# Kernel tuning notes

Measured on AMD Instinct MI355X. Metric: run time of the kernel, lower is better.

## Reference

```python
import jax, jax.numpy as jnp
import numpy as np

N = 100000          # total nodes
E = 1600000         # edges
C = 128             # in_channels
H = 256             # hidden_size
ACT_DIM = 20        # nodes per graph -> batch = N // ACT_DIM


def setup_inputs() -> dict:
    key = jax.random.key(0)
    ks = jax.random.split(key, 10)
    x = jax.random.normal(ks[0], (N, C), dtype=jnp.float32)
    edge_index = jax.random.randint(ks[1], (2, E), 0, N, dtype=jnp.int64)
    s = 0.05
    conv_w = jax.random.normal(ks[2], (C, C), dtype=jnp.float32) * s   # [in, out]
    conv_b = jnp.zeros((C,), dtype=jnp.float32)
    lin1_w = jax.random.normal(ks[3], (H, C), dtype=jnp.float32) * s   # torch [out, in]
    lin1_b = jnp.zeros((H,), dtype=jnp.float32)
    lin2_w = jax.random.normal(ks[4], (H, H), dtype=jnp.float32) * s
    lin2_b = jnp.zeros((H,), dtype=jnp.float32)
    lin3_w = jax.random.normal(ks[5], (1, H), dtype=jnp.float32) * s
    lin3_b = jnp.zeros((1,), dtype=jnp.float32)
    return {"x": x, "edge_index": edge_index,
            "conv_w": conv_w, "conv_b": conv_b,
            "lin1_w": lin1_w, "lin1_b": lin1_b,
            "lin2_w": lin2_w, "lin2_b": lin2_b,
            "lin3_w": lin3_w, "lin3_b": lin3_b}


def gcn_conv(x, edge_index, w, b):
    """PyG GCNConv: x' = D^{-1/2} (A + I) D^{-1/2} (x W) + b."""
    n = x.shape[0]
    loops = jnp.arange(n, dtype=edge_index.dtype)
    src = jnp.concatenate([edge_index[0], loops])  # [E + N]
    dst = jnp.concatenate([edge_index[1], loops])
    deg = jax.ops.segment_sum(jnp.ones_like(dst, dtype=x.dtype), dst, num_segments=n)
    dinv = jnp.where(deg > 0, jax.lax.rsqrt(deg), 0.0)
    norm = dinv[src] * dinv[dst]                   # [E + N]
    xw = x @ w                                     # [N, out]
    msg = xw[src] * norm[:, None]                  # gather + scale, [E+N, out]
    out = jax.ops.segment_sum(msg, dst, num_segments=n)  # scatter-add
    return out + b


def reference(x, edge_index, conv_w, conv_b, lin1_w, lin1_b, lin2_w, lin2_b, lin3_w, lin3_b):
    out = jax.nn.relu(gcn_conv(x, edge_index, conv_w, conv_b))
    h = out + x                                    # residual, [N, C]
    h = h.reshape(-1, ACT_DIM, C)                  # [B, act_dim, C]
    h = jax.nn.relu(h @ lin1_w.T + lin1_b)         # [B, act_dim, H]
    h = jax.nn.relu(h @ lin2_w.T + lin2_b)
    h = jnp.sum(h, axis=1)                         # [B, H]
    h = h @ lin3_w.T + lin3_b                      # [B, 1]
    if h.shape[0] == 1:                            # torch .squeeze(0) semantics
        h = h[0]
    return h
```

## Files before the change

### kernel.cpp

```cpp
#include <hip/hip_runtime.h>
#include <hip/hip_bf16.h>
#include <cstddef>

#define NNODES 100000
#define NEDGES 1600000
#define CIN 128
#define HID 256
#define ACT 20
#define NGRAPH (NNODES / ACT)
#define BSHIFT 8
#define NB ((NNODES + 255) >> 8)
#define BIN_WGS 512
#define PER_WG (NEDGES / BIN_WGS)
#define CAP 8192
#define NSLICE 8
#define PLANE ((size_t)NNODES * 16)

typedef __attribute__((ext_vector_type(8))) short short8;
typedef __attribute__((ext_vector_type(4))) float f32x4;

__device__ __forceinline__ unsigned short f2b(float f) {
    unsigned u = __float_as_uint(f);
    u += 0x7FFF + ((u >> 16) & 1);
    return (unsigned short)(u >> 16);
}
__device__ __forceinline__ float b2f(unsigned short h) {
    return __uint_as_float(((unsigned)h) << 16);
}


__global__ __launch_bounds__(256) void bin_k(const int* __restrict__ ei,
                                             int* __restrict__ bfill,
                                             unsigned* __restrict__ entries) {
    __shared__ int cnt[NB], lofs[NB], base[NB], cur[NB];
    __shared__ unsigned lbuf[PER_WG];
    __shared__ int gdst[PER_WG];
    __shared__ int wsum[4];
    const int t = threadIdx.x;
    for (int i = t; i < NB; i += 256) { cnt[i] = 0; cur[i] = 0; }
    __syncthreads();
    const int s = blockIdx.x * PER_WG;
    const int e = s + PER_WG;
    for (int i = s + t; i < e; i += 256)
        atomicAdd(&cnt[ei[NEDGES + i] >> BSHIFT], 1);
    __syncthreads();
    int c0 = (2 * t < NB) ? cnt[2 * t] : 0;
    int c1 = (2 * t + 1 < NB) ? cnt[2 * t + 1] : 0;
    int v = c0 + c1;
    int lane = t & 63, wid = t >> 6;
    int inc = v;
#pragma unroll
    for (int o = 1; o < 64; o <<= 1) {
        int tv = __shfl_up(inc, o, 64);
        if (lane >= o) inc += tv;
    }
    if (lane == 63) wsum[wid] = inc;
    __syncthreads();
    int woff = 0;
#pragma unroll
    for (int w = 0; w < 4; ++w) woff += (w < wid) ? wsum[w] : 0;
    int excl = inc + woff - v;
    if (2 * t < NB) lofs[2 * t] = excl;
    if (2 * t + 1 < NB) lofs[2 * t + 1] = excl + c0;
    __syncthreads();
    for (int b = t; b < NB; b += 256)
        base[b] = cnt[b] ? atomicAdd(&bfill[b], cnt[b]) : 0;
    __syncthreads();
    for (int i = s + t; i < e; i += 256) {
        int src = ei[i], dst = ei[NEDGES + i];
        int b = dst >> BSHIFT;
        int r = atomicAdd(&cur[b], 1);
        int slot = lofs[b] + r;
        lbuf[slot] = ((unsigned)src << 8) | (unsigned)(dst & 255);
        int g = base[b] + r;
        gdst[slot] = (g < CAP) ? (int)((size_t)b * CAP + g) : -1;
    }
    __syncthreads();
    for (int i = t; i < PER_WG; i += 256) {
        int g = gdst[i];
        if (g >= 0) entries[g] = lbuf[i];
    }
}

__global__ __launch_bounds__(256) void bucket_build_k(
    const unsigned* __restrict__ entries, const int* __restrict__ bfill,
    int2* __restrict__ rowptr2, int* __restrict__ csr, float* __restrict__ dinv) {
    const int b = blockIdx.x;
    const int count = min(bfill[b], CAP);
    const int node0 = b << BSHIFT;
    const int nn = min(256, NNODES - node0);
    const size_t gbase = (size_t)b * CAP;
    __shared__ int cnt[256], off[256], cur[256];
    const int t = threadIdx.x;
    cnt[t] = 0; cur[t] = 0;
    __syncthreads();
    for (int i = t; i < count; i += 256)
        atomicAdd(&cnt[entries[gbase + i] & 255], 1);
    __syncthreads();
    int lane = t & 63, wid = t >> 6;
    int v = cnt[t];
    int inc = v;
#pragma unroll
    for (int o = 1; o < 64; o <<= 1) {
        int tv = __shfl_up(inc, o, 64);
        if (lane >= o) inc += tv;
    }
    __shared__ int wsum[4];
    if (lane == 63) wsum[wid] = inc;
    __syncthreads();
    int woff = 0;
#pragma unroll
    for (int w = 0; w < 4; ++w) woff += (w < wid) ? wsum[w] : 0;
    int excl = inc + woff - v;
    off[t] = excl;
    if (t < nn) {
        rowptr2[node0 + t] = make_int2((int)gbase + excl, (int)gbase + excl + v);
        dinv[node0 + t] = rsqrtf(1.0f + (float)v);
    }
    __syncthreads();
    for (int i = t; i < count; i += 256) {
        unsigned en = entries[gbase + i];
        int loc = (int)(en & 255);
        int r = atomicAdd(&cur[loc], 1);
        csr[gbase + off[loc] + r] = (int)(en >> 8);
    }
}


__global__ void cvt_w_k(const float* __restrict__ conv_w,
                        const float* __restrict__ lin1_w,
                        const float* __restrict__ lin2_w,
                        unsigned short* __restrict__ wt0,
                        unsigned short* __restrict__ wt1,
                        unsigned short* __restrict__ wt2) {
    int id = blockIdx.x * 256 + threadIdx.x;
    if (id < 16384) {
        int k = id >> 7, n = id & 127;
        wt0[n * 128 + k] = f2b(conv_w[k * 128 + n]);
    } else if (id < 16384 + 32768) {
        int i = id - 16384;
        wt1[i] = f2b(lin1_w[i]);
    } else if (id < 16384 + 32768 + 65536) {
        int i = id - 49152;
        wt2[i] = f2b(lin2_w[i]);
    }
}


__global__ __launch_bounds__(256) void mgemm0_k(
    const float* __restrict__ Af, const unsigned short* __restrict__ B,
    const float* __restrict__ dinv, unsigned short* __restrict__ Cout, int M)
{
    const int tid = threadIdx.x;
    const int wid = tid >> 6;
    const int lane = tid & 63;
    const int quad = lane >> 4;
    const int l16 = lane & 15;
    const int bm = blockIdx.x * 128 + (wid >> 1) * 64;
    const int bn = (wid & 1) * 64;

    const float* pa[4];
    const unsigned short* pb[4];
#pragma unroll
    for (int t = 0; t < 4; ++t) {
        int m = bm + t * 16 + l16; if (m >= M) m = M - 1;
        pa[t] = Af + (size_t)m * 128 + quad * 8;
        int n = bn + t * 16 + l16;
        pb[t] = B + (size_t)n * 128 + quad * 8;
    }

    f32x4 acc[4][4];
#pragma unroll
    for (int i = 0; i < 4; ++i)
#pragma unroll
        for (int j = 0; j < 4; ++j) {
            f32x4 z = {0.f, 0.f, 0.f, 0.f};
            acc[i][j] = z;
        }

    float4 afl[2][4][2];
    short8 bf[2][4];
#pragma unroll
    for (int t = 0; t < 4; ++t) {
        afl[0][t][0] = *reinterpret_cast<const float4*>(pa[t]);
        afl[0][t][1] = *reinterpret_cast<const float4*>(pa[t] + 4);
        bf[0][t] = *reinterpret_cast<const short8*>(pb[t]);
    }

#pragma unroll
    for (int kt = 0; kt < 4; ++kt) {
        const int cur = kt & 1, nxt = cur ^ 1;
        if (kt < 3) {
#pragma unroll
            for (int t = 0; t < 4; ++t) {
                afl[nxt][t][0] = *reinterpret_cast<const float4*>(pa[t] + (kt + 1) * 32);
                afl[nxt][t][1] = *reinterpret_cast<const float4*>(pa[t] + (kt + 1) * 32 + 4);
                bf[nxt][t] = *reinterpret_cast<const short8*>(pb[t] + (kt + 1) * 32);
            }
        }
        short8 a[4];
#pragma unroll
        for (int t = 0; t < 4; ++t) {
            float4 f0 = afl[cur][t][0], f1 = afl[cur][t][1];
            short8 av;
            av[0] = (short)f2b(f0.x); av[1] = (short)f2b(f0.y);
            av[2] = (short)f2b(f0.z); av[3] = (short)f2b(f0.w);
            av[4] = (short)f2b(f1.x); av[5] = (short)f2b(f1.y);
            av[6] = (short)f2b(f1.z); av[7] = (short)f2b(f1.w);
            a[t] = av;
        }
#pragma unroll
        for (int i = 0; i < 4; ++i)
#pragma unroll
            for (int j = 0; j < 4; ++j)
                acc[i][j] = __builtin_amdgcn_mfma_f32_16x16x32_bf16(a[i], bf[cur][j], acc[i][j], 0, 0, 0);
    }

#pragma unroll
    for (int i = 0; i < 4; ++i)
#pragma unroll
        for (int r = 0; r < 4; ++r) {
            int row = bm + i * 16 + quad * 4 + r;
            if (row >= M) continue;
            float dv = dinv[row];
#pragma unroll
            for (int j = 0; j < 4; ++j) {
                size_t pbase = (size_t)((bn >> 4) + j) * PLANE;
                Cout[pbase + (size_t)row * 16 + l16] = f2b(acc[i][j][r] * dv);
            }
        }
}


__global__ __launch_bounds__(256) void gather_k(
    const int2* __restrict__ rowptr2, const int* __restrict__ csr,
    const unsigned short* __restrict__ xws, const float* __restrict__ dinv,
    const float* __restrict__ conv_b, unsigned short* __restrict__ h0)
{
    const int slice = blockIdx.x & 7;
    const int ng = blockIdx.x >> 3;
    const int lane = threadIdx.x & 63;
    const int wave = threadIdx.x >> 6;
    const int node = ng * 64 + wave * 16 + (lane >> 2);
    const int cq = lane & 3;
    const int half = cq & 1;
    const int sel = cq >> 1;
    if (node >= NNODES) return;
    const unsigned short* xp = xws + (size_t)slice * PLANE;

    const int2 se = rowptr2[node];
    const int start = se.x, end = se.y;

    float a[8];
    if (cq < 2) {
        uint4 v = *reinterpret_cast<const uint4*>(xp + (size_t)node * 16 + half * 8);
        a[0] = __uint_as_float(v.x << 16); a[1] = __uint_as_float(v.x & 0xffff0000u);
        a[2] = __uint_as_float(v.y << 16); a[3] = __uint_as_float(v.y & 0xffff0000u);
        a[4] = __uint_as_float(v.z << 16); a[5] = __uint_as_float(v.z & 0xffff0000u);
        a[6] = __uint_as_float(v.w << 16); a[7] = __uint_as_float(v.w & 0xffff0000u);
    } else {
#pragma unroll
        for (int i = 0; i < 8; ++i) a[i] = 0.f;
    }

    const int es = start & ~3;
    uint4 nid = *reinterpret_cast<const uint4*>(csr + es);
    for (int e = es; e < end; e += 4) {
        const uint4 idx4 = nid;
        if (e + 4 < end) nid = *reinterpret_cast<const uint4*>(csr + e + 4);
        const int e0 = e + sel, e1 = e + 2 + sel;
        const bool ok0 = (e0 >= start) & (e0 < end);
        const bool ok1 = (e1 >= start) & (e1 < end);
        const int r0 = ok0 ? (sel ? (int)idx4.y : (int)idx4.x) : node;
        const int r1 = ok1 ? (sel ? (int)idx4.w : (int)idx4.z) : node;
        uint4 d0 = *reinterpret_cast<const uint4*>(xp + (size_t)r0 * 16 + half * 8);
        uint4 d1 = *reinterpret_cast<const uint4*>(xp + (size_t)r1 * 16 + half * 8);
        if (ok0) {
            a[0] += __uint_as_float(d0.x << 16); a[1] += __uint_as_float(d0.x & 0xffff0000u);
            a[2] += __uint_as_float(d0.y << 16); a[3] += __uint_as_float(d0.y & 0xffff0000u);
            a[4] += __uint_as_float(d0.z << 16); a[5] += __uint_as_float(d0.z & 0xffff0000u);
            a[6] += __uint_as_float(d0.w << 16); a[7] += __uint_as_float(d0.w & 0xffff0000u);
        }
        if (ok1) {
            a[0] += __uint_as_float(d1.x << 16); a[1] += __uint_as_float(d1.x & 0xffff0000u);
            a[2] += __uint_as_float(d1.y << 16); a[3] += __uint_as_float(d1.y & 0xffff0000u);
            a[4] += __uint_as_float(d1.z << 16); a[5] += __uint_as_float(d1.z & 0xffff0000u);
            a[6] += __uint_as_float(d1.w << 16); a[7] += __uint_as_float(d1.w & 0xffff0000u);
        }
    }

#pragma unroll
    for (int i = 0; i < 8; ++i) a[i] += __shfl_xor(a[i], 2, 64);

    if (cq < 2) {
        const float dv = dinv[node];
        const float4 b0 = *reinterpret_cast<const float4*>(conv_b + slice * 16 + half * 8);
        const float4 b1 = *reinterpret_cast<const float4*>(conv_b + slice * 16 + half * 8 + 4);
        float o[8];
        o[0] = fmaxf(a[0] * dv + b0.x, 0.f);
        o[1] = fmaxf(a[1] * dv + b0.y, 0.f);
        o[2] = fmaxf(a[2] * dv + b0.z, 0.f);
        o[3] = fmaxf(a[3] * dv + b0.w, 0.f);
        o[4] = fmaxf(a[4] * dv + b1.x, 0.f);
        o[5] = fmaxf(a[5] * dv + b1.y, 0.f);
        o[6] = fmaxf(a[6] * dv + b1.z, 0.f);
        o[7] = fmaxf(a[7] * dv + b1.w, 0.f);
        uint4 pk;
        pk.x = (unsigned)f2b(o[0]) | ((unsigned)f2b(o[1]) << 16);
        pk.y = (unsigned)f2b(o[2]) | ((unsigned)f2b(o[3]) << 16);
        pk.z = (unsigned)f2b(o[4]) | ((unsigned)f2b(o[5]) << 16);
        pk.w = (unsigned)f2b(o[6]) | ((unsigned)f2b(o[7]) << 16);
        *reinterpret_cast<uint4*>(h0 + (size_t)slice * PLANE + (size_t)node * 16 + half * 8) = pk;
    }
}


__device__ __forceinline__ short8 addres(short8 h, const float* __restrict__ px) {
    float4 f0 = *reinterpret_cast<const float4*>(px);
    float4 f1 = *reinterpret_cast<const float4*>(px + 4);
    short8 o;
    o[0] = (short)f2b(b2f((unsigned short)h[0]) + f0.x);
    o[1] = (short)f2b(b2f((unsigned short)h[1]) + f0.y);
    o[2] = (short)f2b(b2f((unsigned short)h[2]) + f0.z);
    o[3] = (short)f2b(b2f((unsigned short)h[3]) + f0.w);
    o[4] = (short)f2b(b2f((unsigned short)h[4]) + f1.x);
    o[5] = (short)f2b(b2f((unsigned short)h[5]) + f1.y);
    o[6] = (short)f2b(b2f((unsigned short)h[6]) + f1.z);
    o[7] = (short)f2b(b2f((unsigned short)h[7]) + f1.w);
    return o;
}

__global__ __launch_bounds__(256) void fmlp_k(
    const unsigned short* __restrict__ h0, const float* __restrict__ xres,
    const unsigned short* __restrict__ w1,
    const float* __restrict__ b1, const unsigned short* __restrict__ w2,
    const float* __restrict__ b2, const float* __restrict__ w3,
    float* __restrict__ rowsum, int M)
{
    __shared__ unsigned short h1s[64 * 256];
    const int tid = threadIdx.x;
    const int wave = tid >> 6;
    const int lane = tid & 63;
    const int quad = lane >> 4;
    const int l16 = lane & 15;
    const int bm = blockIdx.x * 64;
    const int nc0 = wave * 64;

    f32x4 acc[4][4];
#pragma unroll
    for (int i = 0; i < 4; ++i)
#pragma unroll
        for (int j = 0; j < 4; ++j) {
            f32x4 z = {0.f, 0.f, 0.f, 0.f};
            acc[i][j] = z;
        }

    {
        const unsigned short* pa[4];
        const float* px[4];
        const unsigned short* pb[4];
#pragma unroll
        for (int t = 0; t < 4; ++t) {
            int m = bm + t * 16 + l16; if (m >= M) m = M - 1;
            pa[t] = h0 + ((size_t)(quad >> 1)) * PLANE + (size_t)m * 16 + (quad & 1) * 8;
            px[t] = xres + (size_t)m * 128 + quad * 8;
            int n = nc0 + t * 16 + l16;
            pb[t] = w1 + (size_t)n * 128 + quad * 8;
        }
        short8 af[2][4], bf[2][4];
#pragma unroll
        for (int t = 0; t < 4; ++t) {
            af[0][t] = addres(*reinterpret_cast<const short8*>(pa[t]), px[t]);
            bf[0][t] = *reinterpret_cast<const short8*>(pb[t]);
        }
#pragma unroll
        for (int kt = 0; kt < 4; ++kt) {
            const int cur = kt & 1, nxt = cur ^ 1;
            if (kt < 3) {
#pragma unroll
                for (int t = 0; t < 4; ++t) {
                    af[nxt][t] = addres(*reinterpret_cast<const short8*>(
                                            pa[t] + (size_t)(kt + 1) * 2 * PLANE),
                                        px[t] + (kt + 1) * 32);
                    bf[nxt][t] = *reinterpret_cast<const short8*>(pb[t] + (kt + 1) * 32);
                }
            }
#pragma unroll
            for (int i = 0; i < 4; ++i)
#pragma unroll
                for (int j = 0; j < 4; ++j)
                    acc[i][j] = __builtin_amdgcn_mfma_f32_16x16x32_bf16(af[cur][i], bf[cur][j], acc[i][j], 0, 0, 0);
        }
#pragma unroll
        for (int nt = 0; nt < 4; ++nt) {
            int col = nc0 + nt * 16 + l16;
            float bv = b1[col];
            int chunk = col >> 3, rem = col & 7;
#pragma unroll
            for (int mt = 0; mt < 4; ++mt)
#pragma unroll
                for (int r = 0; r < 4; ++r) {
                    int row = mt * 16 + quad * 4 + r;
                    h1s[row * 256 + (((chunk ^ (row & 7)) << 3) | rem)] =
                        f2b(fmaxf(acc[mt][nt][r] + bv, 0.f));
                }
        }
    }
    __syncthreads();

#pragma unroll
    for (int i = 0; i < 4; ++i)
#pragma unroll
        for (int j = 0; j < 4; ++j) {
            f32x4 z = {0.f, 0.f, 0.f, 0.f};
            acc[i][j] = z;
        }
    {
        const unsigned short* pb[4];
#pragma unroll
        for (int t = 0; t < 4; ++t) {
            int n = nc0 + t * 16 + l16;
            pb[t] = w2 + (size_t)n * 256 + quad * 8;
        }
        short8 af[3][4], bf[3][4];
#pragma unroll
        for (int t = 0; t < 4; ++t) {
            int row = t * 16 + l16;
            af[0][t] = *reinterpret_cast<const short8*>(
                &h1s[row * 256 + ((quad ^ (row & 7)) << 3)]);
            af[1][t] = *reinterpret_cast<const short8*>(
                &h1s[row * 256 + (((4 + quad) ^ (row & 7)) << 3)]);
            bf[0][t] = *reinterpret_cast<const short8*>(pb[t]);
            bf[1][t] = *reinterpret_cast<const short8*>(pb[t] + 32);
        }
#pragma unroll
        for (int kt = 0; kt < 8; ++kt) {
            const int cu = kt % 3, nx = (kt + 2) % 3;
            if (kt + 2 < 8) {
                const int c2 = (kt + 2) * 4 + quad;
#pragma unroll
                for (int t = 0; t < 4; ++t) {
                    int row = t * 16 + l16;
                    af[nx][t] = *reinterpret_cast<const short8*>(
                        &h1s[row * 256 + ((c2 ^ (row & 7)) << 3)]);
                    bf[nx][t] = *reinterpret_cast<const short8*>(pb[t] + (kt + 2) * 32);
                }
            }
#pragma unroll
            for (int i = 0; i < 4; ++i)
#pragma unroll
                for (int j = 0; j < 4; ++j)
                    acc[i][j] = __builtin_amdgcn_mfma_f32_16x16x32_bf16(af[cu][i], bf[cu][j], acc[i][j], 0, 0, 0);
        }
    }

    float part[4][4];
#pragma unroll
    for (int mt = 0; mt < 4; ++mt)
#pragma unroll
        for (int r = 0; r < 4; ++r) part[mt][r] = 0.f;
#pragma unroll
    for (int nt = 0; nt < 4; ++nt) {
        int col = nc0 + nt * 16 + l16;
        float bs = b2[col];
        float wv3 = w3[col];
#pragma unroll
        for (int mt = 0; mt < 4; ++mt)
#pragma unroll
            for (int r = 0; r < 4; ++r)
                part[mt][r] += fmaxf(acc[mt][nt][r] + bs, 0.f) * wv3;
    }
#pragma unroll
    for (int mt = 0; mt < 4; ++mt)
#pragma unroll
        for (int r = 0; r < 4; ++r) {
            float v = part[mt][r];
            v += __shfl_xor(v, 1, 64);
            v += __shfl_xor(v, 2, 64);
            v += __shfl_xor(v, 4, 64);
            v += __shfl_xor(v, 8, 64);
            part[mt][r] = v;
        }
    if (l16 == 0) {
#pragma unroll
        for (int mt = 0; mt < 4; ++mt)
#pragma unroll
            for (int r = 0; r < 4; ++r) {
                int row = bm + mt * 16 + quad * 4 + r;
                if (row < M) rowsum[(size_t)row * 4 + wave] = part[mt][r];
            }
    }
}


__global__ __launch_bounds__(256) void final_k(
    const float* __restrict__ rowsum, const float* __restrict__ b3,
    float* __restrict__ out)
{
    int g = blockIdx.x * 256 + threadIdx.x;
    if (g >= NGRAPH) return;
    const float4* p = reinterpret_cast<const float4*>(rowsum + (size_t)g * 80);
    float s = 0.f;
#pragma unroll
    for (int i = 0; i < 20; ++i) {
        float4 v = p[i];
        s += (v.x + v.y) + (v.z + v.w);
    }
    out[g] = s + b3[0];
}


extern "C" void kernel_launch(void* const* d_in, const int* in_sizes, int n_in,
                              void* d_out, int out_size, void* d_ws, size_t ws_size,
                              hipStream_t stream)
{
    const float* x      = (const float*)d_in[0];
    const int*   ei     = (const int*)  d_in[1];
    const float* conv_w = (const float*)d_in[2];
    const float* conv_b = (const float*)d_in[3];
    const float* lin1_w = (const float*)d_in[4];
    const float* lin1_b = (const float*)d_in[5];
    const float* lin2_w = (const float*)d_in[6];
    const float* lin2_b = (const float*)d_in[7];
    const float* lin3_w = (const float*)d_in[8];
    const float* lin3_b = (const float*)d_in[9];
    float* out = (float*)d_out;

    unsigned short* xws     = (unsigned short*)d_ws;
    unsigned short* h0      = xws + (size_t)12800000;
    unsigned*       entries = (unsigned*)(h0 + (size_t)12800000);
    int*            csr     = (int*)(entries + (size_t)NB * CAP);
    int2*           rowptr2 = (int2*)(csr + (size_t)NB * CAP);
    float*          dinv    = (float*)(rowptr2 + NNODES);
    int*            bfill   = (int*)(dinv + NNODES);
    unsigned short* wt0     = (unsigned short*)(bfill + NB + 8);
    unsigned short* wt1     = wt0 + 16384;
    unsigned short* wt2     = wt1 + 32768;
    float*          rowsum  = (float*)(wt2 + 65536);

    hipMemsetAsync(bfill, 0, NB * sizeof(int), stream);
    bin_k<<<BIN_WGS, 256, 0, stream>>>(ei, bfill, entries);
    bucket_build_k<<<NB, 256, 0, stream>>>(entries, bfill, rowptr2, csr, dinv);

    cvt_w_k<<<(114688 + 255) / 256, 256, 0, stream>>>(conv_w, lin1_w, lin2_w, wt0, wt1, wt2);

    mgemm0_k<<<(NNODES + 127) / 128, 256, 0, stream>>>(x, wt0, dinv, xws, NNODES);

    gather_k<<<((NNODES + 63) / 64) * NSLICE, 256, 0, stream>>>(rowptr2, csr, xws, dinv,
                                                                conv_b, h0);

    fmlp_k<<<(NNODES + 63) / 64, 256, 0, stream>>>(h0, x, wt1, lin1_b, wt2, lin2_b, lin3_w,
                                                   rowsum, NNODES);

    final_k<<<(NGRAPH + 255) / 256, 256, 0, stream>>>(rowsum, lin3_b, out);
}
```

Baseline: 330.7 us.

## Fuse residual add into gather, pipeline gather loads, merge weight conversion into binning

Folds the bf16 weight conversion into extra workgroups of the binning kernel, which drops one launch, and zeroes a padding row per slice so out-of-range gathers can read a zero sentinel instead of being masked. The gather loop is software-pipelined: the next rows are loaded before the current ones are accumulated, using packed float2 adds. The residual x add moves from the MLP kernel into the gather epilogue, and h0 is now written row-major, so the MLP reads plain bf16 A fragments without reading fp32 x or doing the convert/add per element. The costs are more registers in the gather kernel and a changed rounding point for the residual, which is now rounded once after the add.

Result: no change. 330.4 us (-0.1%).

```diff
diff --git a/kernel.cpp b/kernel.cpp
--- a/kernel.cpp
+++ b/kernel.cpp
@@ -14,28 +14,58 @@
 #define PER_WG (NEDGES / BIN_WGS)
 #define CAP 8192
 #define NSLICE 8
-#define PLANE ((size_t)NNODES * 16)
+#define PROWS (NNODES + 8)
+#define PLANE ((size_t)PROWS * 16)
+#define CVT_WGS 449
 
 typedef __attribute__((ext_vector_type(8))) short short8;
 typedef __attribute__((ext_vector_type(4))) float f32x4;
+typedef __attribute__((ext_vector_type(2))) float f32x2;
 
 __device__ __forceinline__ unsigned short f2b(float f) {
     unsigned u = __float_as_uint(f);
     u += 0x7FFF + ((u >> 16) & 1);
     return (unsigned short)(u >> 16);
 }
-__device__ __forceinline__ float b2f(unsigned short h) {
-    return __uint_as_float(((unsigned)h) << 16);
+__device__ __forceinline__ f32x2 bf2up(unsigned u) {
+    f32x2 r;
+    r.x = __uint_as_float(u << 16);
+    r.y = __uint_as_float(u & 0xffff0000u);
+    return r;
 }
 
 
 __global__ __launch_bounds__(256) void bin_k(const int* __restrict__ ei,
                                              int* __restrict__ bfill,
-                                             unsigned* __restrict__ entries) {
+                                             unsigned* __restrict__ entries,
+                                             const float* __restrict__ conv_w,
+                                             const float* __restrict__ lin1_w,
+                                             const float* __restrict__ lin2_w,
+                                             unsigned short* __restrict__ wt0,
+                                             unsigned short* __restrict__ wt1,
+                                             unsigned short* __restrict__ wt2,
+                                             unsigned short* __restrict__ xws) {
     __shared__ int cnt[NB], lofs[NB], base[NB], cur[NB];
     __shared__ unsigned lbuf[PER_WG];
     __shared__ int gdst[PER_WG];
     __shared__ int wsum[4];
+    if (blockIdx.x >= BIN_WGS) {
+        int id = (blockIdx.x - BIN_WGS) * 256 + threadIdx.x;
+        if (id < 16384) {
+            int k = id >> 7, n = id & 127;
+            wt0[n * 128 + k] = f2b(conv_w[k * 128 + n]);
+        } else if (id < 16384 + 32768) {
+            int i = id - 16384;
+            wt1[i] = f2b(lin1_w[i]);
+        } else if (id < 16384 + 32768 + 65536) {
+            int i = id - 49152;
+            wt2[i] = f2b(lin2_w[i]);
+        } else if (id < 114688 + 128) {
+            int i = id - 114688;
+            xws[(size_t)(i >> 4) * PLANE + (size_t)NNODES * 16 + (i & 15)] = 0;
+        }
+        return;
+    }
     const int t = threadIdx.x;
     for (int i = t; i < NB; i += 256) { cnt[i] = 0; cur[i] = 0; }
     __syncthreads();
@@ -127,26 +157,6 @@
 }
 
 
-__global__ void cvt_w_k(const float* __restrict__ conv_w,
-                        const float* __restrict__ lin1_w,
-                        const float* __restrict__ lin2_w,
-                        unsigned short* __restrict__ wt0,
-                        unsigned short* __restrict__ wt1,
-                        unsigned short* __restrict__ wt2) {
-    int id = blockIdx.x * 256 + threadIdx.x;
-    if (id < 16384) {
-        int k = id >> 7, n = id & 127;
-        wt0[n * 128 + k] = f2b(conv_w[k * 128 + n]);
-    } else if (id < 16384 + 32768) {
-        int i = id - 16384;
-        wt1[i] = f2b(lin1_w[i]);
-    } else if (id < 16384 + 32768 + 65536) {
-        int i = id - 49152;
-        wt2[i] = f2b(lin2_w[i]);
-    }
-}
-
-
 __global__ __launch_bounds__(256) void mgemm0_k(
     const float* __restrict__ Af, const unsigned short* __restrict__ B,
     const float* __restrict__ dinv, unsigned short* __restrict__ Cout, int M)
@@ -235,7 +245,8 @@
 __global__ __launch_bounds__(256) void gather_k(
     const int2* __restrict__ rowptr2, const int* __restrict__ csr,
     const unsigned short* __restrict__ xws, const float* __restrict__ dinv,
-    const float* __restrict__ conv_b, unsigned short* __restrict__ h0)
+    const float* __restrict__ x, const float* __restrict__ conv_b,
+    unsigned short* __restrict__ h0)
 {
     const int slice = blockIdx.x & 7;
     const int ng = blockIdx.x >> 3;
@@ -251,88 +262,79 @@
     const int2 se = rowptr2[node];
     const int start = se.x, end = se.y;
 
-    float a[8];
+    f32x2 a0, a1, a2, a3;
     if (cq < 2) {
         uint4 v = *reinterpret_cast<const uint4*>(xp + (size_t)node * 16 + half * 8);
-        a[0] = __uint_as_float(v.x << 16); a[1] = __uint_as_float(v.x & 0xffff0000u);
-        a[2] = __uint_as_float(v.y << 16); a[3] = __uint_as_float(v.y & 0xffff0000u);
-        a[4] = __uint_as_float(v.z << 16); a[5] = __uint_as_float(v.z & 0xffff0000u);
-        a[6] = __uint_as_float(v.w << 16); a[7] = __uint_as_float(v.w & 0xffff0000u);
+        a0 = bf2up(v.x); a1 = bf2up(v.y); a2 = bf2up(v.z); a3 = bf2up(v.w);
     } else {
-#pragma unroll
-        for (int i = 0; i < 8; ++i) a[i] = 0.f;
+        f32x2 z = {0.f, 0.f};
+        a0 = z; a1 = z; a2 = z; a3 = z;
     }
 
     const int es = start & ~3;
-    uint4 nid = *reinterpret_cast<const uint4*>(csr + es);
-    for (int e = es; e < end; e += 4) {
-        const uint4 idx4 = nid;
-        if (e + 4 < end) nid = *reinterpret_cast<const uint4*>(csr + e + 4);
-        const int e0 = e + sel, e1 = e + 2 + sel;
-        const bool ok0 = (e0 >= start) & (e0 < end);
-        const bool ok1 = (e1 >= start) & (e1 < end);
-        const int r0 = ok0 ? (sel ? (int)idx4.y : (int)idx4.x) : node;
-        const int r1 = ok1 ? (sel ? (int)idx4.w : (int)idx4.z) : node;
-        uint4 d0 = *reinterpret_cast<const uint4*>(xp + (size_t)r0 * 16 + half * 8);
-        uint4 d1 = *reinterpret_cast<const uint4*>(xp + (size_t)r1 * 16 + half * 8);
-        if (ok0) {
-            a[0] += __uint_as_float(d0.x << 16); a[1] += __uint_as_float(d0.x & 0xffff0000u);
-            a[2] += __uint_as_float(d0.y << 16); a[3] += __uint_as_float(d0.y & 0xffff0000u);
-            a[4] += __uint_as_float(d0.z << 16); a[5] += __uint_as_float(d0.z & 0xffff0000u);
-            a[6] += __uint_as_float(d0.w << 16); a[7] += __uint_as_float(d0.w & 0xffff0000u);
-        }
-        if (ok1) {
-            a[0] += __uint_as_float(d1.x << 16); a[1] += __uint_as_float(d1.x & 0xffff0000u);
-            a[2] += __uint_as_float(d1.y << 16); a[3] += __uint_as_float(d1.y & 0xffff0000u);
-            a[4] += __uint_as_float(d1.z << 16); a[5] += __uint_as_float(d1.z & 0xffff0000u);
-            a[6] += __uint_as_float(d1.w << 16); a[7] += __uint_as_float(d1.w & 0xffff0000u);
-        }
-    }
-
-#pragma unroll
-    for (int i = 0; i < 8; ++i) a[i] += __shfl_xor(a[i], 2, 64);
+    const int nsteps = (end - es + 3) >> 2;
+
+    uint4 inext;
+    uint4 dc0, dc1;
+    if (nsteps > 0) {
+        uint4 i0 = *reinterpret_cast<const uint4*>(csr + es);
+        int e0 = es + sel, e1 = es + 2 + sel;
+        int r0 = (e0 >= start && e0 < end) ? (sel ? (int)i0.y : (int)i0.x) : NNODES;
+        int r1 = (e1 >= start && e1 < end) ? (sel ? (int)i0.w : (int)i0.z) : NNODES;
+        dc0 = *reinterpret_cast<const uint4*>(xp + (size_t)r0 * 16 + half * 8);
+        dc1 = *reinterpret_cast<const uint4*>(xp + (size_t)r1 * 16 + half * 8);
+        if (nsteps > 1) inext = *reinterpret_cast<const uint4*>(csr + es + 4);
+    }
+    for (int s = 0; s < nsteps; ++s) {
+        const int e = es + s * 4;
+        uint4 dn0, dn1;
+        if (s + 1 < nsteps) {
+            const int en0 = e + 4 + sel, en1 = e + 6 + sel;
+            int rn0 = (en0 < end) ? (sel ? (int)inext.y : (int)inext.x) : NNODES;
+            int rn1 = (en1 < end) ? (sel ? (int)inext.w : (int)inext.z) : NNODES;
+            dn0 = *reinterpret_cast<const uint4*>(xp + (size_t)rn0 * 16 + half * 8);
+            dn1 = *reinterpret_cast<const uint4*>(xp + (size_t)rn1 * 16 + half * 8);
+        }
+        if (s + 2 < nsteps)
+            inext = *reinterpret_cast<const uint4*>(csr + e + 8);
+        a0 += bf2up(dc0.x); a1 += bf2up(dc0.y); a2 += bf2up(dc0.z); a3 += bf2up(dc0.w);
+        a0 += bf2up(dc1.x); a1 += bf2up(dc1.y); a2 += bf2up(dc1.z); a3 += bf2up(dc1.w);
+        dc0 = dn0; dc1 = dn1;
+    }
+
+    float av[8] = {a0.x, a0.y, a1.x, a1.y, a2.x, a2.y, a3.x, a3.y};
+#pragma unroll
+    for (int i = 0; i < 8; ++i) av[i] += __shfl_xor(av[i], 2, 64);
 
     if (cq < 2) {
         const float dv = dinv[node];
-        const float4 b0 = *reinterpret_cast<const float4*>(conv_b + slice * 16 + half * 8);
-        const float4 b1 = *reinterpret_cast<const float4*>(conv_b + slice * 16 + half * 8 + 4);
+        const float* bb = conv_b + slice * 16 + half * 8;
+        const float4 b0 = *reinterpret_cast<const float4*>(bb);
+        const float4 b1 = *reinterpret_cast<const float4*>(bb + 4);
+        const float* xr = x + (size_t)node * 128 + slice * 16 + half * 8;
+        const float4 x0 = *reinterpret_cast<const float4*>(xr);
+        const float4 x1 = *reinterpret_cast<const float4*>(xr + 4);
         float o[8];
-        o[0] = fmaxf(a[0] * dv + b0.x, 0.f);
-        o[1] = fmaxf(a[1] * dv + b0.y, 0.f);
-        o[2] = fmaxf(a[2] * dv + b0.z, 0.f);
-        o[3] = fmaxf(a[3] * dv + b0.w, 0.f);
-        o[4] = fmaxf(a[4] * dv + b1.x, 0.f);
-        o[5] = fmaxf(a[5] * dv + b1.y, 0.f);
-        o[6] = fmaxf(a[6] * dv + b1.z, 0.f);
-        o[7] = fmaxf(a[7] * dv + b1.w, 0.f);
+        o[0] = fmaxf(av[0] * dv + b0.x, 0.f) + x0.x;
+        o[1] = fmaxf(av[1] * dv + b0.y, 0.f) + x0.y;
+        o[2] = fmaxf(av[2] * dv + b0.z, 0.f) + x0.z;
+        o[3] = fmaxf(av[3] * dv + b0.w, 0.f) + x0.w;
+        o[4] = fmaxf(av[4] * dv + b1.x, 0.f) + x1.x;
+        o[5] = fmaxf(av[5] * dv + b1.y, 0.f) + x1.y;
+        o[6] = fmaxf(av[6] * dv + b1.z, 0.f) + x1.z;
+        o[7] = fmaxf(av[7] * dv + b1.w, 0.f) + x1.w;
         uint4 pk;
         pk.x = (unsigned)f2b(o[0]) | ((unsigned)f2b(o[1]) << 16);
         pk.y = (unsigned)f2b(o[2]) | ((unsigned)f2b(o[3]) << 16);
         pk.z = (unsigned)f2b(o[4]) | ((unsigned)f2b(o[5]) << 16);
         pk.w = (unsigned)f2b(o[6]) | ((unsigned)f2b(o[7]) << 16);
-        *reinterpret_cast<uint4*>(h0 + (size_t)slice * PLANE + (size_t)node * 16 + half * 8) = pk;
-    }
-}
-
-
-__device__ __forceinline__ short8 addres(short8 h, const float* __restrict__ px) {
-    float4 f0 = *reinterpret_cast<const float4*>(px);
-    float4 f1 = *reinterpret_cast<const float4*>(px + 4);
-    short8 o;
-    o[0] = (short)f2b(b2f((unsigned short)h[0]) + f0.x);
-    o[1] = (short)f2b(b2f((unsigned short)h[1]) + f0.y);
-    o[2] = (short)f2b(b2f((unsigned short)h[2]) + f0.z);
-    o[3] = (short)f2b(b2f((unsigned short)h[3]) + f0.w);
-    o[4] = (short)f2b(b2f((unsigned short)h[4]) + f1.x);
-    o[5] = (short)f2b(b2f((unsigned short)h[5]) + f1.y);
-    o[6] = (short)f2b(b2f((unsigned short)h[6]) + f1.z);
-    o[7] = (short)f2b(b2f((unsigned short)h[7]) + f1.w);
-    return o;
-}
+        *reinterpret_cast<uint4*>(h0 + (size_t)node * CIN + slice * 16 + half * 8) = pk;
+    }
+}
+
 
 __global__ __launch_bounds__(256) void fmlp_k(
-    const unsigned short* __restrict__ h0, const float* __restrict__ xres,
-    const unsigned short* __restrict__ w1,
+    const unsigned short* __restrict__ h0, const unsigned short* __restrict__ w1,
     const float* __restrict__ b1, const unsigned short* __restrict__ w2,
     const float* __restrict__ b2, const float* __restrict__ w3,
     float* __restrict__ rowsum, int M)
@@ -357,20 +359,18 @@
 
     {
         const unsigned short* pa[4];
-        const float* px[4];
         const unsigned short* pb[4];
 #pragma unroll
         for (int t = 0; t < 4; ++t) {
             int m = bm + t * 16 + l16; if (m >= M) m = M - 1;
-            pa[t] = h0 + ((size_t)(quad >> 1)) * PLANE + (size_t)m * 16 + (quad & 1) * 8;
-            px[t] = xres + (size_t)m * 128 + quad * 8;
+            pa[t] = h0 + (size_t)m * 128 + quad * 8;
             int n = nc0 + t * 16 + l16;
             pb[t] = w1 + (size_t)n * 128 + quad * 8;
         }
         short8 af[2][4], bf[2][4];
 #pragma unroll
         for (int t = 0; t < 4; ++t) {
-            af[0][t] = addres(*reinterpret_cast<const short8*>(pa[t]), px[t]);
+            af[0][t] = *reinterpret_cast<const short8*>(pa[t]);
             bf[0][t] = *reinterpret_cast<const short8*>(pb[t]);
         }
 #pragma unroll
@@ -379,9 +379,7 @@
             if (kt < 3) {
 #pragma unroll
                 for (int t = 0; t < 4; ++t) {
-                    af[nxt][t] = addres(*reinterpret_cast<const short8*>(
-                                            pa[t] + (size_t)(kt + 1) * 2 * PLANE),
-                                        px[t] + (kt + 1) * 32);
+                    af[nxt][t] = *reinterpret_cast<const short8*>(pa[t] + (kt + 1) * 32);
                     bf[nxt][t] = *reinterpret_cast<const short8*>(pb[t] + (kt + 1) * 32);
                 }
             }
@@ -527,7 +525,7 @@
     float* out = (float*)d_out;
 
     unsigned short* xws     = (unsigned short*)d_ws;
-    unsigned short* h0      = xws + (size_t)12800000;
+    unsigned short* h0      = xws + (size_t)NSLICE * PLANE;
     unsigned*       entries = (unsigned*)(h0 + (size_t)12800000);
     int*            csr     = (int*)(entries + (size_t)NB * CAP);
     int2*           rowptr2 = (int2*)(csr + (size_t)NB * CAP);
@@ -539,17 +537,17 @@
     float*          rowsum  = (float*)(wt2 + 65536);
 
     hipMemsetAsync(bfill, 0, NB * sizeof(int), stream);
-    bin_k<<<BIN_WGS, 256, 0, stream>>>(ei, bfill, entries);
+    bin_k<<<BIN_WGS + CVT_WGS, 256, 0, stream>>>(ei, bfill, entries,
+                                                 conv_w, lin1_w, lin2_w,
+                                                 wt0, wt1, wt2, xws);
     bucket_build_k<<<NB, 256, 0, stream>>>(entries, bfill, rowptr2, csr, dinv);
 
-    cvt_w_k<<<(114688 + 255) / 256, 256, 0, stream>>>(conv_w, lin1_w, lin2_w, wt0, wt1, wt2);
-
     mgemm0_k<<<(NNODES + 127) / 128, 256, 0, stream>>>(x, wt0, dinv, xws, NNODES);
 
     gather_k<<<((NNODES + 63) / 64) * NSLICE, 256, 0, stream>>>(rowptr2, csr, xws, dinv,
-                                                                conv_b, h0);
-
-    fmlp_k<<<(NNODES + 63) / 64, 256, 0, stream>>>(h0, x, wt1, lin1_b, wt2, lin2_b, lin3_w,
+                                                                x, conv_b, h0);
+
+    fmlp_k<<<(NNODES + 63) / 64, 256, 0, stream>>>(h0, wt1, lin1_b, wt2, lin2_b, lin3_w,
                                                    rowsum, NNODES);
 
     final_k<<<(NGRAPH + 255) / 256, 256, 0, stream>>>(rowsum, lin3_b, out);
```
